# Kernel optimization log

Measured on AMD Instinct MI355X. Metric: run time of the kernel, lower is better.

## Reference

```python
import jax, jax.numpy as jnp
import numpy as np

B, L_DEC, V = 8, 256, 32000
L_SRC = 512
V_EXT = 32128


def setup_inputs() -> dict:
    key = jax.random.key(0)
    k1, k2, k3, k4 = jax.random.split(key, 4)
    dist_t = jax.random.uniform(k1, (B, L_DEC, V), dtype=jnp.float32)
    p_gen = jax.random.uniform(k2, (B, L_DEC, 1), dtype=jnp.float32)
    alph_t = jax.random.uniform(k3, (B, L_SRC, L_DEC), dtype=jnp.float32)
    batch_vocab = jnp.zeros((V_EXT,), dtype=jnp.float32)  # only shape[0] is used
    pointer = jax.random.randint(k4, (B, L_SRC), 0, V_EXT, dtype=jnp.int32)
    return {"dist_t": dist_t, "p_gen": p_gen, "alph_t": alph_t,
            "batch_vocab": batch_vocab, "pointer": pointer}


def reference(dist_t, p_gen, alph_t, batch_vocab, pointer):
    v_ext = batch_vocab.shape[0]
    nb, nl, ndim = dist_t.shape
    # p_gen * [vocab ; zeros padding up to extended vocab]
    prob_vocab = p_gen * jnp.pad(dist_t, ((0, 0), (0, 0), (0, v_ext - ndim)))
    # torch builds a dense one-hot [B, L_src, V_ext] and does bmm(alpha^T, one_hot).
    # Mathematically: copyp[b, t, v] = sum_{s : pointer[b,s]==v} alpha[b, s, t]
    # -> scatter-add of attention weights into pointed vocab slots.
    alpha_td = jnp.swapaxes(alph_t, 1, 2)  # [B, L_dec, L_src]

    def scatter_one(a_td, ptr):  # a_td: [L_dec, L_src], ptr: [L_src]
        return jnp.zeros((a_td.shape[0], v_ext), a_td.dtype).at[:, ptr].add(a_td)

    copyp = jax.vmap(scatter_one)(alpha_td, pointer)  # [B, L_dec, V_ext]
    proba = prob_vocab + (1.0 - p_gen) * copyp
    return proba
```

## Files before the change

kernel.cpp:

```cpp
#include <hip/hip_runtime.h>

#define B_     8
#define L_DEC_ 256
#define V_     32000
#define L_SRC_ 512
#define V_EXT_ 32128

#define V4_    (V_ / 4)
#define VE4_   (V_EXT_ / 4)
#define NITER_ ((VE4_ + 511) / 512)

typedef float f32x4 __attribute__((ext_vector_type(4)));

__global__ __launch_bounds__(512, 8) void copynet_fused(
    const float* __restrict__ dist,
    const float* __restrict__ p_gen,
    const float* __restrict__ alph,
    const int*   __restrict__ pointer,
    float* __restrict__ out)
{
    __shared__ int   head[512];
    __shared__ int   nxt[512];
    __shared__ int   key[512];
    __shared__ float sval[512];

    const int row = blockIdx.x;
    const int b   = row >> 8;
    const int t   = row & (L_DEC_ - 1);
    const int tid = threadIdx.x;

    const float pg   = p_gen[row];
    const float coef = 1.0f - pg;

    const int   sIdx = b * L_SRC_ + tid;
    const int   v    = pointer[sIdx];
    const float val  = coef * alph[(size_t)sIdx * L_DEC_ + t];

    head[tid] = -1;
    __syncthreads();
    key[tid]  = v;
    sval[tid] = val;
    const int owner = (v >> 2) & 511;
    nxt[tid] = atomicExch(&head[owner], tid);
    __syncthreads();

    const int myHead = head[tid];
    const f32x4* dist4 = (const f32x4*)(dist + (size_t)row * V_);
    f32x4*       out4  = (f32x4*)(out + (size_t)row * V_EXT_);

    for (int k = 0; k < NITER_; ++k) {
        const int i = tid + (k << 9);
        if (i >= VE4_) break;
        f32x4 r;
        if (i < V4_) {
            r = __builtin_nontemporal_load(dist4 + i) * pg;
        } else {
            r = (f32x4){0.f, 0.f, 0.f, 0.f};
        }
        for (int e = myHead; e != -1; e = nxt[e]) {
            const int kv = key[e];
            if ((kv >> 2) == i) {
                const float a = sval[e];
                const int   c = kv & 3;
                r.x += (c == 0) ? a : 0.f;
                r.y += (c == 1) ? a : 0.f;
                r.z += (c == 2) ? a : 0.f;
                r.w += (c == 3) ? a : 0.f;
            }
        }
        __builtin_nontemporal_store(r, out4 + i);
    }
}

extern "C" void kernel_launch(void* const* d_in, const int* in_sizes, int n_in,
                              void* d_out, int out_size, void* d_ws, size_t ws_size,
                              hipStream_t stream)
{
    const float* dist    = (const float*)d_in[0];
    const float* p_gen   = (const float*)d_in[1];
    const float* alph    = (const float*)d_in[2];
    const int*   pointer = (const int*)d_in[4];
    float* out = (float*)d_out;

    copynet_fused<<<B_ * L_DEC_, 512, 0, stream>>>(dist, p_gen, alph, pointer, out);
}
```

Before: 439.4 us.

## Process four decoder rows per block and skip empty pointer chains via bitmask

Each block now handles four consecutive decoder positions. It builds the pointer hash chain once and reuses it across the four rows, and it loads alpha and p_gen as float4 vectors instead of scalars. A per-thread bitmask records which 512-wide chunks hold matching keys, so chain traversal is skipped for chunks that cannot match. The cost is a quarter as many blocks, which lowers parallelism, and the launch-bounds occupancy hint is removed.

```diff
diff --git a/kernel.cpp b/kernel.cpp
--- a/kernel.cpp
+++ b/kernel.cpp
@@ -8,11 +8,12 @@
 
 #define V4_    (V_ / 4)
 #define VE4_   (V_EXT_ / 4)
-#define NITER_ ((VE4_ + 511) / 512)
+
+#define ROWS_  4
 
 typedef float f32x4 __attribute__((ext_vector_type(4)));
 
-__global__ __launch_bounds__(512, 8) void copynet_fused(
+__global__ __launch_bounds__(512) void copynet_fused(
     const float* __restrict__ dist,
     const float* __restrict__ p_gen,
     const float* __restrict__ alph,
@@ -22,53 +23,64 @@
     __shared__ int   head[512];
     __shared__ int   nxt[512];
     __shared__ int   key[512];
-    __shared__ float sval[512];
+    __shared__ float sval[ROWS_][512];
 
-    const int row = blockIdx.x;
-    const int b   = row >> 8;
-    const int t   = row & (L_DEC_ - 1);
+    const int bid = blockIdx.x;
+    const int b   = bid >> 6;
+    const int t0  = (bid & 63) << 2;
     const int tid = threadIdx.x;
 
-    const float pg   = p_gen[row];
-    const float coef = 1.0f - pg;
+    const f32x4 pgv = *(const f32x4*)(p_gen + b * L_DEC_ + t0);
 
     const int   sIdx = b * L_SRC_ + tid;
     const int   v    = pointer[sIdx];
-    const float val  = coef * alph[(size_t)sIdx * L_DEC_ + t];
+    const f32x4 av   = *(const f32x4*)(alph + (size_t)sIdx * L_DEC_ + t0);
 
     head[tid] = -1;
     __syncthreads();
-    key[tid]  = v;
-    sval[tid] = val;
-    const int owner = (v >> 2) & 511;
-    nxt[tid] = atomicExch(&head[owner], tid);
+    key[tid]     = v;
+    sval[0][tid] = (1.0f - pgv.x) * av.x;
+    sval[1][tid] = (1.0f - pgv.y) * av.y;
+    sval[2][tid] = (1.0f - pgv.z) * av.z;
+    sval[3][tid] = (1.0f - pgv.w) * av.w;
+    nxt[tid] = atomicExch(&head[(v >> 2) & 511], tid);
     __syncthreads();
 
     const int myHead = head[tid];
-    const f32x4* dist4 = (const f32x4*)(dist + (size_t)row * V_);
-    f32x4*       out4  = (f32x4*)(out + (size_t)row * V_EXT_);
+    unsigned mask = 0u;
+    for (int e = myHead; e != -1; e = nxt[e])
+        mask |= 1u << (key[e] >> 11);
 
-    for (int k = 0; k < NITER_; ++k) {
-        const int i = tid + (k << 9);
-        if (i >= VE4_) break;
-        f32x4 r;
-        if (i < V4_) {
-            r = __builtin_nontemporal_load(dist4 + i) * pg;
-        } else {
-            r = (f32x4){0.f, 0.f, 0.f, 0.f};
+#pragma unroll
+    for (int r = 0; r < ROWS_; ++r) {
+        const int row = b * L_DEC_ + t0 + r;
+        const float pg = (r == 0) ? pgv.x : (r == 1) ? pgv.y
+                                          : (r == 2) ? pgv.z : pgv.w;
+        const f32x4* dist4 = (const f32x4*)(dist + (size_t)row * V_);
+        f32x4*       out4  = (f32x4*)(out + (size_t)row * V_EXT_);
+
+        for (int i = tid; i < VE4_; i += 512) {
+            f32x4 rr;
+            if (i < V4_) {
+                rr = __builtin_nontemporal_load(dist4 + i) * pg;
+            } else {
+                rr = (f32x4){0.f, 0.f, 0.f, 0.f};
+            }
+            if (mask & (1u << (i >> 9))) {
+                for (int e = myHead; e != -1; e = nxt[e]) {
+                    const int kv = key[e];
+                    if ((kv >> 2) == i) {
+                        const float a = sval[r][e];
+                        const int   c = kv & 3;
+                        rr.x += (c == 0) ? a : 0.f;
+                        rr.y += (c == 1) ? a : 0.f;
+                        rr.z += (c == 2) ? a : 0.f;
+                        rr.w += (c == 3) ? a : 0.f;
+                    }
+                }
+            }
+            __builtin_nontemporal_store(rr, out4 + i);
         }
-        for (int e = myHead; e != -1; e = nxt[e]) {
-            const int kv = key[e];
-            if ((kv >> 2) == i) {
-                const float a = sval[e];
-                const int   c = kv & 3;
-                r.x += (c == 0) ? a : 0.f;
-                r.y += (c == 1) ? a : 0.f;
-                r.z += (c == 2) ? a : 0.f;
-                r.w += (c == 3) ? a : 0.f;
-            }
-        }
-        __builtin_nontemporal_store(r, out4 + i);
     }
 }
 
@@ -82,5 +94,6 @@
     const int*   pointer = (const int*)d_in[4];
     float* out = (float*)d_out;
 
-    copynet_fused<<<B_ * L_DEC_, 512, 0, stream>>>(dist, p_gen, alph, pointer, out);
+    copynet_fused<<<B_ * (L_DEC_ / ROWS_), 512, 0, stream>>>(
+        dist, p_gen, alph, pointer, out);
 }
```

Result: no change. 443.6 us (+1.0%).
